# Performance work log

Measured on AMD Instinct MI355X. Metric: run time of the kernel, lower is better.

The kernel has to match this reference:

```python
import jax, jax.numpy as jnp
import numpy as np

B, L, D = 16, 1024, 768

def setup_inputs() -> dict:
    key = jax.random.key(0)
    ks = jax.random.split(key, 6)
    s = 1.0 / np.sqrt(D)  # torch Linear default init scale
    return {
        "h": jax.random.normal(ks[0], (B, L, D), dtype=jnp.float32),
        "q": jax.random.normal(ks[1], (B, L, D), dtype=jnp.float32),
        "w1_w": jax.random.uniform(ks[2], (L, D), jnp.float32, -s, s),
        "w1_b": jax.random.uniform(ks[3], (L,), jnp.float32, -s, s),
        "w2_w": jax.random.uniform(ks[4], (L, D), jnp.float32, -s, s),
        "w2_b": jax.random.uniform(ks[5], (L,), jnp.float32, -s, s),
    }

def reference(h, q, w1_w, w1_b, w2_w, w2_b):
    # w1h: [B, L, l], w2q: [B, L, l] -> permuted [B, l, L]
    w1h = jnp.einsum('bsd,ld->bsl', h, w1_w) + w1_b
    w2q = jnp.einsum('btd,ld->btl', q, w2_w) + w2_b
    w3hq = jnp.einsum('bsd,btd->bst', h, q)           # [B, L, L]
    a = w1h + jnp.swapaxes(w2q, 1, 2) + w3hq          # [B, L, L]
    p = jax.nn.softmax(a, axis=2)
    c = jnp.einsum('bst,btd->bsd', p, q)              # [B, L, D]
    m = jnp.max(a, axis=2)                            # [B, L]
    p2 = jax.nn.softmax(m, axis=1)                    # [B, L]
    qc = h * p2[:, :, None]                           # [B, L, D]
    return jnp.concatenate([h, c, h * c, qc * c], axis=2)  # [B, L, 4D]
```

## Files before the change

kernel.cpp:

```cpp
#include <hip/hip_runtime.h>
#include <stdint.h>

#define B_  16
#define L_  1024
#define D_  768
#define K1_ 1536

typedef unsigned short u16;
typedef __attribute__((ext_vector_type(4))) float f32x4;
typedef __attribute__((ext_vector_type(8))) _Float16 f16x8;

__device__ __forceinline__ u16 f2h(float x){
    return __builtin_bit_cast(u16, (_Float16)x);
}
__device__ __forceinline__ float h2f(u16 x){
    return (float)__builtin_bit_cast(_Float16, x);
}

__device__ __forceinline__ void gload_lds16(const void* g, void* l){
    __builtin_amdgcn_global_load_lds((const __attribute__((address_space(1))) void*)g,
                                     (__attribute__((address_space(3))) void*)l, 16, 0, 0);
}

__global__ __launch_bounds__(256) void prep(const float* __restrict__ h, const float* __restrict__ q,
    const float* __restrict__ w1w, const float* __restrict__ w2w,
    u16* __restrict__ hH, u16* __restrict__ wH, u16* __restrict__ qH,
    u16* __restrict__ w1h, u16* __restrict__ qT, int b0, int nb)
{
    __shared__ float tile[32][33];
    int bb = blockIdx.z, bg = b0 + bb;
    int t0 = blockIdx.x * 32, d0 = blockIdx.y * 32;
    int tid = threadIdx.x;
    int r  = tid >> 3;
    int c4 = (tid & 7) * 4;
    int t = t0 + r, d = d0 + c4;
    size_t goff = (size_t)t * D_ + d;

    float4 qv  = *(const float4*)(q   + (size_t)bg * L_ * D_ + goff);
    float4 hv  = *(const float4*)(h   + (size_t)bg * L_ * D_ + goff);
    float4 w2v = *(const float4*)(w2w + goff);

    tile[r][c4 + 0] = qv.x; tile[r][c4 + 1] = qv.y;
    tile[r][c4 + 2] = qv.z; tile[r][c4 + 3] = qv.w;

    size_t o = ((size_t)bb * L_ + t) * D_ + d;
    ushort4 a;
    a.x = f2h(hv.x); a.y = f2h(hv.y); a.z = f2h(hv.z); a.w = f2h(hv.w);
    *(ushort4*)(hH + o) = a;
    a.x = f2h(hv.x + w2v.x); a.y = f2h(hv.y + w2v.y);
    a.z = f2h(hv.z + w2v.z); a.w = f2h(hv.w + w2v.w);
    *(ushort4*)(wH + o) = a;
    a.x = f2h(qv.x); a.y = f2h(qv.y); a.z = f2h(qv.z); a.w = f2h(qv.w);
    *(ushort4*)(qH + o) = a;
    if (bb == 0){
        float4 w1v = *(const float4*)(w1w + goff);
        a.x = f2h(w1v.x); a.y = f2h(w1v.y); a.z = f2h(w1v.z); a.w = f2h(w1v.w);
        *(ushort4*)(w1h + goff) = a;
    }
    __syncthreads();
    int dr = tid >> 3;
    int tc = (tid & 7) * 4;
    ushort4 b;
    b.x = f2h(tile[tc + 0][dr]); b.y = f2h(tile[tc + 1][dr]);
    b.z = f2h(tile[tc + 2][dr]); b.w = f2h(tile[tc + 3][dr]);
    *(ushort4*)(qT + (size_t)bb * D_ * L_ + (size_t)(d0 + dr) * L_ + t0 + tc) = b;
}

__global__ __launch_bounds__(256) void gemm1(
    const u16* __restrict__ hH, const u16* __restrict__ wH,
    const u16* __restrict__ qH, const u16* __restrict__ w1h,
    const float* __restrict__ w1b, const float* __restrict__ w2b,
    u16* __restrict__ aH)
{
    __shared__ u16 ldsA[128 * 64];
    __shared__ u16 ldsB[128 * 64];
    int nwg = gridDim.x;
    int o = blockIdx.x;
    int wg = (o & 7) * (nwg >> 3) + (o >> 3);
    int bb = wg >> 6;
    int tl = wg & 63;
    int sm = tl >> 3, tn = tl & 7;
    int s0 = sm * 128, t0 = tn * 128;
    int tid = threadIdx.x;
    int lane = tid & 63, wid = tid >> 6;
    int wm = wid >> 1, wn = wid & 1;
    int l15 = lane & 15, l4 = lane >> 4;

    const u16* hHb = hH + (size_t)bb * L_ * D_;
    const u16* wHb = wH + (size_t)bb * L_ * D_;
    const u16* qHb = qH + (size_t)bb * L_ * D_;

    f32x4 acc[4][4];
    #pragma unroll
    for (int m = 0; m < 4; m++)
        #pragma unroll
        for (int n = 0; n < 4; n++)
            acc[m][n] = (f32x4){0.f, 0.f, 0.f, 0.f};

    for (int kb = 0; kb < K1_; kb += 64){
        bool inH = (kb < D_);
        const u16* Asrc = inH ? hHb : wHb;
        const u16* Bsrc = inH ? w1h : qHb;
        int koff = inH ? kb : (kb - D_);
        #pragma unroll
        for (int j = 0; j < 4; j++){
            int n = j * 256 + tid;
            int row = n >> 3, c = n & 7;
            int cc = c ^ (row & 7);
            int k = koff + cc * 8;
            gload_lds16(Asrc + (size_t)(s0 + row) * D_ + k, &ldsA[(j * 256 + wid * 64) * 8]);
            gload_lds16(Bsrc + (size_t)(t0 + row) * D_ + k, &ldsB[(j * 256 + wid * 64) * 8]);
        }
        __syncthreads();
        #pragma unroll
        for (int kk = 0; kk < 2; kk++){
            f16x8 af[4], bf[4];
            #pragma unroll
            for (int m = 0; m < 4; m++){
                int row = wm * 64 + m * 16 + l15;
                int c = kk * 4 + l4;
                af[m] = *(const f16x8*)&ldsA[(row * 8 + (c ^ (row & 7))) * 8];
            }
            #pragma unroll
            for (int n = 0; n < 4; n++){
                int row = wn * 64 + n * 16 + l15;
                int c = kk * 4 + l4;
                bf[n] = *(const f16x8*)&ldsB[(row * 8 + (c ^ (row & 7))) * 8];
            }
            #pragma unroll
            for (int m = 0; m < 4; m++)
                #pragma unroll
                for (int n = 0; n < 4; n++)
                    acc[m][n] = __builtin_amdgcn_mfma_f32_16x16x32_f16(af[m], bf[n], acc[m][n], 0, 0, 0);
        }
        __syncthreads();
    }

    u16* aRow = aH + (size_t)bb * L_ * L_;
    #pragma unroll
    for (int n = 0; n < 4; n++){
        int tcol = t0 + wn * 64 + n * 16 + l15;
        float w1v = w1b[tcol];
        #pragma unroll
        for (int m = 0; m < 4; m++){
            int sbase = s0 + wm * 64 + m * 16 + l4 * 4;
            #pragma unroll
            for (int r = 0; r < 4; r++){
                int s = sbase + r;
                aRow[(size_t)s * L_ + tcol] = f2h(acc[m][n][r] + w1v + w2b[s]);
            }
        }
    }
}

__global__ __launch_bounds__(256) void rowsm(const u16* __restrict__ aH, u16* __restrict__ pB,
                                             float* __restrict__ mws, int b0)
{
    __shared__ float red[4];
    int rowid = blockIdx.x;
    int bb = rowid >> 10, s = rowid & 1023;
    const u16* row = aH + (size_t)rowid * L_;
    int tid = threadIdx.x;
    ushort4 pv = ((const ushort4*)row)[tid];
    float v0 = h2f(pv.x), v1 = h2f(pv.y), v2 = h2f(pv.z), v3 = h2f(pv.w);
    float mx = fmaxf(fmaxf(v0, v1), fmaxf(v2, v3));
    #pragma unroll
    for (int o = 32; o; o >>= 1) mx = fmaxf(mx, __shfl_xor(mx, o));
    if ((tid & 63) == 0) red[tid >> 6] = mx;
    __syncthreads();
    mx = fmaxf(fmaxf(red[0], red[1]), fmaxf(red[2], red[3]));
    float e0 = __expf(v0 - mx), e1 = __expf(v1 - mx), e2 = __expf(v2 - mx), e3 = __expf(v3 - mx);
    float sum = e0 + e1 + e2 + e3;
    #pragma unroll
    for (int o = 32; o; o >>= 1) sum += __shfl_xor(sum, o);
    __syncthreads();
    if ((tid & 63) == 0) red[tid >> 6] = sum;
    __syncthreads();
    sum = red[0] + red[1] + red[2] + red[3];
    float inv = 1.0f / sum;
    ushort4 pk;
    pk.x = f2h(e0 * inv); pk.y = f2h(e1 * inv); pk.z = f2h(e2 * inv); pk.w = f2h(e3 * inv);
    ((ushort4*)(pB + (size_t)rowid * L_))[tid] = pk;
    if (tid == 0) mws[(size_t)(b0 + bb) * L_ + s] = mx;
}

__global__ __launch_bounds__(1024) void p2k(const float* __restrict__ mws, float* __restrict__ p2, int b0)
{
    __shared__ float red[16];
    int bg = b0 + blockIdx.x;
    int tid = threadIdx.x;
    float v = mws[(size_t)bg * L_ + tid];
    float mx = v;
    #pragma unroll
    for (int o = 32; o; o >>= 1) mx = fmaxf(mx, __shfl_xor(mx, o));
    if ((tid & 63) == 0) red[tid >> 6] = mx;
    __syncthreads();
    float m2 = red[0];
    #pragma unroll
    for (int i = 1; i < 16; i++) m2 = fmaxf(m2, red[i]);
    float e = __expf(v - m2);
    float sum = e;
    #pragma unroll
    for (int o = 32; o; o >>= 1) sum += __shfl_xor(sum, o);
    __syncthreads();
    if ((tid & 63) == 0) red[tid >> 6] = sum;
    __syncthreads();
    float st = 0.f;
    #pragma unroll
    for (int i = 0; i < 16; i++) st += red[i];
    p2[(size_t)bg * L_ + tid] = e / st;
}

__global__ __launch_bounds__(256) void gemm2(const u16* __restrict__ pB, const u16* __restrict__ qT,
    float* __restrict__ cB)
{
    __shared__ u16 ldsA[128 * 64];
    __shared__ u16 ldsB[128 * 64];
    int nwg = gridDim.x;
    int o = blockIdx.x;
    int wg = (o & 7) * (nwg >> 3) + (o >> 3);
    int bb = wg / 48;
    int tl = wg % 48;
    int sm = tl / 6, dn = tl % 6;
    int s0 = sm * 128, d0 = dn * 128;
    int tid = threadIdx.x;
    int lane = tid & 63, wid = tid >> 6;
    int wm = wid >> 1, wn = wid & 1;
    int l15 = lane & 15, l4 = lane >> 4;

    const u16* Ab = pB + (size_t)bb * L_ * L_;
    const u16* Bb = qT + (size_t)bb * D_ * L_;

    f32x4 acc[4][4];
    #pragma unroll
    for (int m = 0; m < 4; m++)
        #pragma unroll
        for (int n = 0; n < 4; n++)
            acc[m][n] = (f32x4){0.f, 0.f, 0.f, 0.f};

    for (int kb = 0; kb < L_; kb += 64){
        #pragma unroll
        for (int j = 0; j < 4; j++){
            int n = j * 256 + tid;
            int row = n >> 3, c = n & 7;
            int cc = c ^ (row & 7);
            gload_lds16(Ab + (size_t)(s0 + row) * L_ + kb + cc * 8, &ldsA[(j * 256 + wid * 64) * 8]);
        }
        #pragma unroll
        for (int j = 0; j < 4; j++){
            int n = j * 256 + tid;
            int row = n >> 3, c = n & 7;
            int cc = c ^ (row & 7);
            gload_lds16(Bb + (size_t)(d0 + row) * L_ + kb + cc * 8, &ldsB[(j * 256 + wid * 64) * 8]);
        }
        __syncthreads();
        #pragma unroll
        for (int kk = 0; kk < 2; kk++){
            f16x8 af[4], bf[4];
            #pragma unroll
            for (int m = 0; m < 4; m++){
                int row = wm * 64 + m * 16 + l15;
                int c = kk * 4 + l4;
                af[m] = *(const f16x8*)&ldsA[(row * 8 + (c ^ (row & 7))) * 8];
            }
            #pragma unroll
            for (int n = 0; n < 4; n++){
                int row = wn * 64 + n * 16 + l15;
                int c = kk * 4 + l4;
                bf[n] = *(const f16x8*)&ldsB[(row * 8 + (c ^ (row & 7))) * 8];
            }
            #pragma unroll
            for (int m = 0; m < 4; m++)
                #pragma unroll
                for (int n = 0; n < 4; n++)
                    acc[m][n] = __builtin_amdgcn_mfma_f32_16x16x32_f16(af[m], bf[n], acc[m][n], 0, 0, 0);
        }
        __syncthreads();
    }

    float* cRow = cB + (size_t)bb * L_ * D_;
    #pragma unroll
    for (int m = 0; m < 4; m++){
        int sbase = s0 + wm * 64 + m * 16 + l4 * 4;
        #pragma unroll
        for (int r = 0; r < 4; r++){
            int s = sbase + r;
            #pragma unroll
            for (int n = 0; n < 4; n++){
                int d = d0 + wn * 64 + n * 16 + l15;
                cRow[(size_t)s * D_ + d] = acc[m][n][r];
            }
        }
    }
}

__global__ __launch_bounds__(192) void epi(const float* __restrict__ cB, const float* __restrict__ h,
    const float* __restrict__ p2, float* __restrict__ out, int b0)
{
    int rowid = blockIdx.x;
    int bb = rowid >> 10, s = rowid & 1023;
    int bg = b0 + bb;
    float p2v = p2[(size_t)bg * L_ + s];
    const float* cR = cB + (size_t)rowid * D_;
    const float* hR = h + ((size_t)bg * L_ + s) * D_;
    float* oR = out + ((size_t)bg * L_ + s) * (4 * D_);
    int d = threadIdx.x * 4;
    float4 cv = *(const float4*)(cR + d);
    float4 hv = *(const float4*)(hR + d);
    float4 hc = {hv.x * cv.x, hv.y * cv.y, hv.z * cv.z, hv.w * cv.w};
    float4 qc = {p2v * hc.x, p2v * hc.y, p2v * hc.z, p2v * hc.w};
    *(float4*)(oR + d)          = hv;
    *(float4*)(oR + D_ + d)     = cv;
    *(float4*)(oR + 2 * D_ + d) = hc;
    *(float4*)(oR + 3 * D_ + d) = qc;
}

extern "C" void kernel_launch(void* const* d_in, const int* in_sizes, int n_in,
                              void* d_out, int out_size, void* d_ws, size_t ws_size,
                              hipStream_t stream)
{
    const float* h   = (const float*)d_in[0];
    const float* q   = (const float*)d_in[1];
    const float* w1w = (const float*)d_in[2];
    const float* w1b = (const float*)d_in[3];
    const float* w2w = (const float*)d_in[4];
    const float* w2b = (const float*)d_in[5];
    float* out = (float*)d_out;

    const size_t szPlane = (size_t)L_ * D_ * 2;
    const size_t szM     = (size_t)B_ * L_ * 4;
    const size_t perB_aH = (size_t)L_ * L_ * 2;
    const size_t perB_pB = (size_t)L_ * L_ * 2;
    const size_t perB_cB = (size_t)L_ * D_ * 4;
    const size_t perB = 4 * szPlane + perB_aH + perB_pB + perB_cB;
    const size_t fixed = szPlane + 2 * szM;

    int NB = 1;
    if (ws_size > fixed){
        size_t nbc = (ws_size - fixed) / perB;
        NB = (nbc >= 16) ? 16 : (nbc < 1 ? 1 : (int)nbc);
    }

    char* p = (char*)d_ws;
    u16*   w1h  = (u16*)p;   p += szPlane;
    float* mws  = (float*)p; p += szM;
    float* p2   = (float*)p; p += szM;
    u16*   hH   = (u16*)p;   p += szPlane * NB;
    u16*   wH   = (u16*)p;   p += szPlane * NB;
    u16*   qH   = (u16*)p;   p += szPlane * NB;
    u16*   qT   = (u16*)p;   p += szPlane * NB;
    u16*   pB   = (u16*)p;   p += perB_pB * NB;
    float* cB   = (float*)p; p += perB_cB * NB;
    u16*   aH   = (u16*)p;

    for (int b0 = 0; b0 < B_; b0 += NB){
        int nb = (B_ - b0 < NB) ? (B_ - b0) : NB;
        prep  <<<dim3(32, 24, nb), 256, 0, stream>>>(h, q, w1w, w2w, hH, wH, qH, w1h, qT, b0, nb);
        gemm1 <<<dim3(64 * nb), 256, 0, stream>>>(hH, wH, qH, w1h, w1b, w2b, aH);
        rowsm <<<dim3(nb * 1024), 256, 0, stream>>>(aH, pB, mws, b0);
        p2k   <<<dim3(nb), 1024, 0, stream>>>(mws, p2, b0);
        gemm2 <<<dim3(48 * nb), 256, 0, stream>>>(pB, qT, cB);
        epi   <<<dim3(nb * 1024), 192, 0, stream>>>(cB, h, p2, out, b0);
    }
}
```

Before: 227.4 us.

## Fuse row-max into gemm1 epilogue and write gemm2 output directly into result

gemm1 now computes per-tile partial row maxima of the logits and writes them to a small buffer. p2k reduces those partials into the full row max and runs before rowsm, so rowsm drops its max reduction and one barrier. gemm2 writes c straight into its slot in the output, and epi reads it back from there, which removes the separate cB buffer and one store pass. The row max is now taken from fp32 values before the fp16 rounding of the stored logits, so it can differ very slightly from the max of the stored values.

```diff
diff --git a/kernel.cpp b/kernel.cpp
--- a/kernel.cpp
+++ b/kernel.cpp
@@ -70,7 +70,7 @@
     const u16* __restrict__ hH, const u16* __restrict__ wH,
     const u16* __restrict__ qH, const u16* __restrict__ w1h,
     const float* __restrict__ w1b, const float* __restrict__ w2b,
-    u16* __restrict__ aH)
+    u16* __restrict__ aH, float* __restrict__ mT)
 {
     __shared__ u16 ldsA[128 * 64];
     __shared__ u16 ldsB[128 * 64];
@@ -138,42 +138,77 @@
 
     u16* aRow = aH + (size_t)bb * L_ * L_;
     #pragma unroll
-    for (int n = 0; n < 4; n++){
-        int tcol = t0 + wn * 64 + n * 16 + l15;
-        float w1v = w1b[tcol];
-        #pragma unroll
-        for (int m = 0; m < 4; m++){
-            int sbase = s0 + wm * 64 + m * 16 + l4 * 4;
-            #pragma unroll
-            for (int r = 0; r < 4; r++){
-                int s = sbase + r;
-                aRow[(size_t)s * L_ + tcol] = f2h(acc[m][n][r] + w1v + w2b[s]);
-            }
-        }
-    }
+    for (int m = 0; m < 4; m++){
+        #pragma unroll
+        for (int r = 0; r < 4; r++){
+            int s = s0 + wm * 64 + m * 16 + l4 * 4 + r;
+            float w2v = w2b[s];
+            float tmax = -1e30f;
+            #pragma unroll
+            for (int n = 0; n < 4; n++){
+                int tcol = t0 + wn * 64 + n * 16 + l15;
+                float v = acc[m][n][r] + w1b[tcol] + w2v;
+                aRow[(size_t)s * L_ + tcol] = f2h(v);
+                tmax = fmaxf(tmax, v);
+            }
+            #pragma unroll
+            for (int o2 = 1; o2 < 16; o2 <<= 1)
+                tmax = fmaxf(tmax, __shfl_xor(tmax, o2));
+            if (l15 == 0)
+                mT[((size_t)bb * L_ + s) * 16 + tn * 2 + wn] = tmax;
+        }
+    }
+}
+
+__global__ __launch_bounds__(1024) void p2k(const float* __restrict__ mT, float* __restrict__ mws,
+                                            float* __restrict__ p2, int b0)
+{
+    __shared__ float red[16];
+    int bb = blockIdx.x, bg = b0 + bb;
+    int tid = threadIdx.x;
+    const float4* rowv = (const float4*)(mT + ((size_t)bb * L_ + tid) * 16);
+    float4 a0 = rowv[0], a1 = rowv[1], a2 = rowv[2], a3 = rowv[3];
+    float v = fmaxf(fmaxf(fmaxf(a0.x, a0.y), fmaxf(a0.z, a0.w)),
+             fmaxf(fmaxf(fmaxf(a1.x, a1.y), fmaxf(a1.z, a1.w)),
+             fmaxf(fmaxf(fmaxf(a2.x, a2.y), fmaxf(a2.z, a2.w)),
+                   fmaxf(fmaxf(a3.x, a3.y), fmaxf(a3.z, a3.w)))));
+    mws[(size_t)bg * L_ + tid] = v;
+    float mx = v;
+    #pragma unroll
+    for (int o = 32; o; o >>= 1) mx = fmaxf(mx, __shfl_xor(mx, o));
+    if ((tid & 63) == 0) red[tid >> 6] = mx;
+    __syncthreads();
+    float m2 = red[0];
+    #pragma unroll
+    for (int i = 1; i < 16; i++) m2 = fmaxf(m2, red[i]);
+    float e = __expf(v - m2);
+    float sum = e;
+    #pragma unroll
+    for (int o = 32; o; o >>= 1) sum += __shfl_xor(sum, o);
+    __syncthreads();
+    if ((tid & 63) == 0) red[tid >> 6] = sum;
+    __syncthreads();
+    float st = 0.f;
+    #pragma unroll
+    for (int i = 0; i < 16; i++) st += red[i];
+    p2[(size_t)bg * L_ + tid] = e / st;
 }
 
 __global__ __launch_bounds__(256) void rowsm(const u16* __restrict__ aH, u16* __restrict__ pB,
-                                             float* __restrict__ mws, int b0)
+                                             const float* __restrict__ mws, int b0)
 {
     __shared__ float red[4];
     int rowid = blockIdx.x;
     int bb = rowid >> 10, s = rowid & 1023;
+    float mx = mws[(size_t)(b0 + bb) * L_ + s];
     const u16* row = aH + (size_t)rowid * L_;
     int tid = threadIdx.x;
     ushort4 pv = ((const ushort4*)row)[tid];
-    float v0 = h2f(pv.x), v1 = h2f(pv.y), v2 = h2f(pv.z), v3 = h2f(pv.w);
-    float mx = fmaxf(fmaxf(v0, v1), fmaxf(v2, v3));
-    #pragma unroll
-    for (int o = 32; o; o >>= 1) mx = fmaxf(mx, __shfl_xor(mx, o));
-    if ((tid & 63) == 0) red[tid >> 6] = mx;
-    __syncthreads();
-    mx = fmaxf(fmaxf(red[0], red[1]), fmaxf(red[2], red[3]));
-    float e0 = __expf(v0 - mx), e1 = __expf(v1 - mx), e2 = __expf(v2 - mx), e3 = __expf(v3 - mx);
+    float e0 = __expf(h2f(pv.x) - mx), e1 = __expf(h2f(pv.y) - mx);
+    float e2 = __expf(h2f(pv.z) - mx), e3 = __expf(h2f(pv.w) - mx);
     float sum = e0 + e1 + e2 + e3;
     #pragma unroll
     for (int o = 32; o; o >>= 1) sum += __shfl_xor(sum, o);
-    __syncthreads();
     if ((tid & 63) == 0) red[tid >> 6] = sum;
     __syncthreads();
     sum = red[0] + red[1] + red[2] + red[3];
@@ -181,38 +216,10 @@
     ushort4 pk;
     pk.x = f2h(e0 * inv); pk.y = f2h(e1 * inv); pk.z = f2h(e2 * inv); pk.w = f2h(e3 * inv);
     ((ushort4*)(pB + (size_t)rowid * L_))[tid] = pk;
-    if (tid == 0) mws[(size_t)(b0 + bb) * L_ + s] = mx;
-}
-
-__global__ __launch_bounds__(1024) void p2k(const float* __restrict__ mws, float* __restrict__ p2, int b0)
-{
-    __shared__ float red[16];
-    int bg = b0 + blockIdx.x;
-    int tid = threadIdx.x;
-    float v = mws[(size_t)bg * L_ + tid];
-    float mx = v;
-    #pragma unroll
-    for (int o = 32; o; o >>= 1) mx = fmaxf(mx, __shfl_xor(mx, o));
-    if ((tid & 63) == 0) red[tid >> 6] = mx;
-    __syncthreads();
-    float m2 = red[0];
-    #pragma unroll
-    for (int i = 1; i < 16; i++) m2 = fmaxf(m2, red[i]);
-    float e = __expf(v - m2);
-    float sum = e;
-    #pragma unroll
-    for (int o = 32; o; o >>= 1) sum += __shfl_xor(sum, o);
-    __syncthreads();
-    if ((tid & 63) == 0) red[tid >> 6] = sum;
-    __syncthreads();
-    float st = 0.f;
-    #pragma unroll
-    for (int i = 0; i < 16; i++) st += red[i];
-    p2[(size_t)bg * L_ + tid] = e / st;
 }
 
 __global__ __launch_bounds__(256) void gemm2(const u16* __restrict__ pB, const u16* __restrict__ qT,
-    float* __restrict__ cB)
+    float* __restrict__ out, int b0)
 {
     __shared__ u16 ldsA[128 * 64];
     __shared__ u16 ldsB[128 * 64];
@@ -278,7 +285,7 @@
         __syncthreads();
     }
 
-    float* cRow = cB + (size_t)bb * L_ * D_;
+    float* oC = out + ((size_t)(b0 + bb) * L_) * (4 * D_) + D_;
     #pragma unroll
     for (int m = 0; m < 4; m++){
         int sbase = s0 + wm * 64 + m * 16 + l4 * 4;
@@ -288,29 +295,27 @@
             #pragma unroll
             for (int n = 0; n < 4; n++){
                 int d = d0 + wn * 64 + n * 16 + l15;
-                cRow[(size_t)s * D_ + d] = acc[m][n][r];
-            }
-        }
-    }
-}
-
-__global__ __launch_bounds__(192) void epi(const float* __restrict__ cB, const float* __restrict__ h,
+                oC[(size_t)s * (4 * D_) + d] = acc[m][n][r];
+            }
+        }
+    }
+}
+
+__global__ __launch_bounds__(192) void epi(const float* __restrict__ h,
     const float* __restrict__ p2, float* __restrict__ out, int b0)
 {
     int rowid = blockIdx.x;
     int bb = rowid >> 10, s = rowid & 1023;
     int bg = b0 + bb;
     float p2v = p2[(size_t)bg * L_ + s];
-    const float* cR = cB + (size_t)rowid * D_;
     const float* hR = h + ((size_t)bg * L_ + s) * D_;
     float* oR = out + ((size_t)bg * L_ + s) * (4 * D_);
     int d = threadIdx.x * 4;
-    float4 cv = *(const float4*)(cR + d);
+    float4 cv = *(const float4*)(oR + D_ + d);
     float4 hv = *(const float4*)(hR + d);
     float4 hc = {hv.x * cv.x, hv.y * cv.y, hv.z * cv.z, hv.w * cv.w};
     float4 qc = {p2v * hc.x, p2v * hc.y, p2v * hc.z, p2v * hc.w};
     *(float4*)(oR + d)          = hv;
-    *(float4*)(oR + D_ + d)     = cv;
     *(float4*)(oR + 2 * D_ + d) = hc;
     *(float4*)(oR + 3 * D_ + d) = qc;
 }
@@ -331,8 +336,8 @@
     const size_t szM     = (size_t)B_ * L_ * 4;
     const size_t perB_aH = (size_t)L_ * L_ * 2;
     const size_t perB_pB = (size_t)L_ * L_ * 2;
-    const size_t perB_cB = (size_t)L_ * D_ * 4;
-    const size_t perB = 4 * szPlane + perB_aH + perB_pB + perB_cB;
+    const size_t perB_mT = (size_t)L_ * 16 * 4;
+    const size_t perB = 4 * szPlane + perB_aH + perB_pB + perB_mT;
     const size_t fixed = szPlane + 2 * szM;
 
     int NB = 1;
@@ -345,21 +350,21 @@
     u16*   w1h  = (u16*)p;   p += szPlane;
     float* mws  = (float*)p; p += szM;
     float* p2   = (float*)p; p += szM;
+    float* mT   = (float*)p; p += perB_mT * NB;
     u16*   hH   = (u16*)p;   p += szPlane * NB;
     u16*   wH   = (u16*)p;   p += szPlane * NB;
     u16*   qH   = (u16*)p;   p += szPlane * NB;
     u16*   qT   = (u16*)p;   p += szPlane * NB;
     u16*   pB   = (u16*)p;   p += perB_pB * NB;
-    float* cB   = (float*)p; p += perB_cB * NB;
     u16*   aH   = (u16*)p;
 
     for (int b0 = 0; b0 < B_; b0 += NB){
         int nb = (B_ - b0 < NB) ? (B_ - b0) : NB;
         prep  <<<dim3(32, 24, nb), 256, 0, stream>>>(h, q, w1w, w2w, hH, wH, qH, w1h, qT, b0, nb);
-        gemm1 <<<dim3(64 * nb), 256, 0, stream>>>(hH, wH, qH, w1h, w1b, w2b, aH);
+        gemm1 <<<dim3(64 * nb), 256, 0, stream>>>(hH, wH, qH, w1h, w1b, w2b, aH, mT);
+        p2k   <<<dim3(nb), 1024, 0, stream>>>(mT, mws, p2, b0);
         rowsm <<<dim3(nb * 1024), 256, 0, stream>>>(aH, pB, mws, b0);
-        p2k   <<<dim3(nb), 1024, 0, stream>>>(mws, p2, b0);
-        gemm2 <<<dim3(48 * nb), 256, 0, stream>>>(pB, qT, cB);
-        epi   <<<dim3(nb * 1024), 192, 0, stream>>>(cB, h, p2, out, b0);
-    }
-}
+        gemm2 <<<dim3(48 * nb), 256, 0, stream>>>(pB, qT, out, b0);
+        epi   <<<dim3(nb * 1024), 192, 0, stream>>>(h, p2, out, b0);
+    }
+}
```

Result: no change. 231.1 us (+1.6%).
